# Kernel optimization log

Hardware: AMD Instinct MI355X
Metric: run time of the kernel (lower is better)

The kernel has to match this reference:

```python
import jax, jax.numpy as jnp
import numpy as np
import math

H = 16  # num heads
NEG = -1e9


def setup_inputs() -> dict:
    key = jax.random.key(0)
    ks = jax.random.split(key, 12)
    B, S, D = 2, 2048, 1024
    inp = {
        "query": jax.random.normal(ks[0], (B, S, D), jnp.float32),
        "key": jax.random.normal(ks[1], (B, S, D), jnp.float32),
        "value": jax.random.normal(ks[2], (B, S, D), jnp.float32),
        "mask": jax.random.randint(ks[3], (B, 1, S), 0, 2, jnp.int32),
        "wq": jax.random.normal(ks[4], (D, D), jnp.float32) * 0.02,
        "bq": jnp.zeros((D,), jnp.float32),
        "wk": jax.random.normal(ks[5], (D, D), jnp.float32) * 0.02,
        "bk": jnp.zeros((D,), jnp.float32),
        "wv": jax.random.normal(ks[6], (D, D), jnp.float32) * 0.02,
        "bv": jnp.zeros((D,), jnp.float32),
        "wo": jax.random.normal(ks[7], (D, D), jnp.float32) * 0.02,
        "bo": jnp.zeros((D,), jnp.float32),
    }
    return inp


def reference(query, key, value, mask, wq, bq, wk, bk, wv, bv, wo, bo):
    B, S, D = query.shape
    dk = D // H

    def proj(x, w, b):
        # torch Linear: x @ w.T + b ; then split heads -> [B, H, S, dk]
        y = x @ w.T + b
        return y.reshape(B, -1, H, dk).transpose(0, 2, 1, 3)

    q = proj(query, wq, bq)
    k = proj(key, wk, bk)
    v = proj(value, wv, bv)

    scores = jnp.einsum("bhqd,bhkd->bhqk", q, k) / math.sqrt(dk)  # [B,H,S,S]

    m = mask[:, None, :, :]  # [B,1,1,S] (mask.unsqueeze(1) in torch)
    scores = jnp.where(m == 0, NEG, scores)            # key-side padding mask
    scores = jnp.where(jnp.swapaxes(m, -2, -1) == 0, NEG, scores)  # query-side mask (q_len>1)

    p_attn = jax.nn.softmax(scores, axis=-1)
    # dropout p=0 / eval mode -> identity
    ctx = jnp.einsum("bhqk,bhkd->bhqd", p_attn, v)  # [B,H,S,dk]
    ctx = ctx.transpose(0, 2, 1, 3).reshape(B, S, H * dk)
    out = ctx @ wo.T + bo
    return out
```

## Files before the change

### kernel.cpp

```cpp
#include <hip/hip_runtime.h>
#include <hip/hip_bf16.h>

#define SEQ 2048
#define DIM 1024
#define NH  16
#define DK  64
#define NA  (2 * SEQ * DIM)
#define NW  (DIM * DIM)
#define PSTR 72
#define ESTR 136
#define FSTR 132
#define QSCALE 0.18033688011112042f

typedef __attribute__((ext_vector_type(4))) float f32x4;
typedef __attribute__((ext_vector_type(8))) __bf16 bf16x8;
typedef __attribute__((ext_vector_type(4))) __bf16 bf16x4;

__device__ __forceinline__ f32x4 mfma16(bf16x8 a, bf16x8 b, f32x4 c) {
  return __builtin_amdgcn_mfma_f32_16x16x32_bf16(a, b, c, 0, 0, 0);
}
__device__ __forceinline__ void async_load16(const void* g, void* l) {
  __builtin_amdgcn_global_load_lds(
      (const __attribute__((address_space(1))) void*)g,
      (__attribute__((address_space(3))) void*)l, 16, 0, 0);
}
__device__ __forceinline__ int swz(int row, int chunk) {
  return row * 8 + (chunk ^ (row & 7));
}

__global__ __launch_bounds__(256) void cvt_kernel(
    const float* __restrict__ s0, const float* __restrict__ s1,
    const float* __restrict__ s2, const float* __restrict__ s3,
    const float* __restrict__ s4, const float* __restrict__ s5,
    const float* __restrict__ s6,
    __hip_bfloat16* __restrict__ d0, __hip_bfloat16* __restrict__ d1,
    __hip_bfloat16* __restrict__ d2, __hip_bfloat16* __restrict__ d3,
    __hip_bfloat16* __restrict__ d4, __hip_bfloat16* __restrict__ d5,
    __hip_bfloat16* __restrict__ d6) {
  const int id = blockIdx.x;
  const float* s;
  __hip_bfloat16* d;
  int bid;
  if (id < 6144) {
    int t = id >> 11;
    bid = id & 2047;
    s = (t == 0) ? s0 : ((t == 1) ? s1 : s2);
    d = (t == 0) ? d0 : ((t == 1) ? d1 : d2);
  } else {
    int t = (id - 6144) >> 9;
    bid = (id - 6144) & 511;
    s = (t == 0) ? s3 : ((t == 1) ? s4 : ((t == 2) ? s5 : s6));
    d = (t == 0) ? d3 : ((t == 1) ? d4 : ((t == 2) ? d5 : d6));
  }
  size_t i = ((size_t)bid * 256 + threadIdx.x) * 8;
  float4 a = *(const float4*)(s + i);
  float4 b = *(const float4*)(s + i + 4);
  bf16x8 v = {(__bf16)a.x, (__bf16)a.y, (__bf16)a.z, (__bf16)a.w,
              (__bf16)b.x, (__bf16)b.y, (__bf16)b.z, (__bf16)b.w};
  *(bf16x8*)(d + i) = v;
}

__device__ __forceinline__ void gemm_mainloop(
    const __hip_bfloat16* __restrict__ X, const __hip_bfloat16* __restrict__ W,
    __hip_bfloat16* A_lds, __hip_bfloat16* B_lds, int m0, int n0,
    f32x4 acc[4][4]) {
  const int K = DIM;
  const int tid = threadIdx.x, lane = tid & 63, w = tid >> 6;
  const int quad = lane >> 4, l15 = lane & 15;
  const int wm = (w >> 1) * 64, wn = (w & 1) * 64;

  f32x4 z = {0.f, 0.f, 0.f, 0.f};
  for (int mi = 0; mi < 4; ++mi)
    for (int ni = 0; ni < 4; ++ni) acc[mi][ni] = z;

  for (int k0 = 0; k0 < K; k0 += 64) {
    for (int r = 0; r < 4; ++r) {
      int cbase = r * 256 + w * 64;
      int c = cbase + lane, row = c >> 3, cs = c & 7;
      int off = cs ^ (row & 7);
      async_load16((const char*)(X + (size_t)(m0 + row) * K + k0) + off * 16,
                   (char*)A_lds + cbase * 16);
      async_load16((const char*)(W + (size_t)(n0 + row) * K + k0) + off * 16,
                   (char*)B_lds + cbase * 16);
    }
    __syncthreads();
    for (int kk = 0; kk < 2; ++kk) {
      bf16x8 a[4], b[4];
      for (int mi = 0; mi < 4; ++mi)
        a[mi] = *(const bf16x8*)(A_lds + swz(wm + mi * 16 + l15, kk * 4 + quad) * 8);
      for (int ni = 0; ni < 4; ++ni)
        b[ni] = *(const bf16x8*)(B_lds + swz(wn + ni * 16 + l15, kk * 4 + quad) * 8);
      for (int mi = 0; mi < 4; ++mi)
        for (int ni = 0; ni < 4; ++ni)
          acc[mi][ni] = mfma16(a[mi], b[ni], acc[mi][ni]);
    }
    __syncthreads();
  }
}

__global__ __launch_bounds__(256) void qkv_proj_kernel(
    const __hip_bfloat16* __restrict__ xq, const __hip_bfloat16* __restrict__ xk,
    const __hip_bfloat16* __restrict__ xv,
    const __hip_bfloat16* __restrict__ wq, const __hip_bfloat16* __restrict__ wk,
    const __hip_bfloat16* __restrict__ wv,
    const float* __restrict__ bq, const float* __restrict__ bk,
    const float* __restrict__ bv,
    __hip_bfloat16* __restrict__ q_ws, __hip_bfloat16* __restrict__ k_ws,
    __hip_bfloat16* __restrict__ vt_ws) {
  __shared__ __align__(16) __hip_bfloat16 S_lds[128 * ESTR];

  const int z = blockIdx.z;
  const __hip_bfloat16* X = (z == 0) ? xq : ((z == 1) ? xk : xv);
  const __hip_bfloat16* W = (z == 0) ? wq : ((z == 1) ? wk : wv);
  const float* bias = (z == 0) ? bq : ((z == 1) ? bk : bv);
  const float f = (z == 0) ? QSCALE : 1.0f;

  const int m0 = blockIdx.y * 128, n0 = blockIdx.x * 128;
  f32x4 acc[4][4];
  gemm_mainloop(X, W, S_lds, S_lds + 128 * 64, m0, n0, acc);

  const int tid = threadIdx.x, lane = tid & 63, w = tid >> 6;
  const int quad = lane >> 4, l15 = lane & 15;
  const int wm = (w >> 1) * 64, wn = (w & 1) * 64;

  if (z != 2) {
    __hip_bfloat16* out = (z == 0) ? q_ws : k_ws;
    for (int p = 0; p < 2; ++p) {
      if ((w >> 1) == p) {
        for (int mi = 0; mi < 4; ++mi)
          for (int ni = 0; ni < 4; ++ni) {
            const float bv_ = bias[n0 + wn + ni * 16 + l15];
            for (int r = 0; r < 4; ++r)
              S_lds[(mi * 16 + quad * 4 + r) * ESTR + wn + ni * 16 + l15] =
                  __float2bfloat16((acc[mi][ni][r] + bv_) * f);
          }
      }
      __syncthreads();
      for (int r2 = 0; r2 < 4; ++r2) {
        int c = r2 * 256 + tid;
        int row = c >> 4, j = c & 15;
        int m = m0 + p * 64 + row, b = m >> 11, s = m & 2047;
        int n = n0 + j * 8, h = n >> 6, d = n & 63;
        *(uint4*)(out + ((size_t)(b * NH + h) * SEQ + s) * DK + d) =
            *(const uint4*)(S_lds + row * ESTR + j * 8);
      }
      __syncthreads();
    }
  } else {
    for (int mi = 0; mi < 4; ++mi)
      for (int ni = 0; ni < 4; ++ni) {
        const int n_local = wn + ni * 16 + l15;
        const float bv_ = bias[n0 + n_local];
        bf16x4 tv;
        for (int r = 0; r < 4; ++r) tv[r] = (__bf16)(acc[mi][ni][r] + bv_);
        *(bf16x4*)(S_lds + n_local * ESTR + wm + mi * 16 + quad * 4) = tv;
      }
    __syncthreads();
    const int b = m0 >> 11, s_base = m0 & 2047;
    for (int r2 = 0; r2 < 8; ++r2) {
      int c2 = r2 * 256 + tid;
      int nrow = c2 >> 4, moff = (c2 & 15) * 8;
      int n = n0 + nrow, h = n >> 6, d = n & 63;
      *(uint4*)(vt_ws + ((size_t)(b * NH + h) * DK + d) * SEQ + s_base + moff) =
          *(const uint4*)(S_lds + nrow * ESTR + moff);
    }
  }
}

__global__ __launch_bounds__(512) void attn_kernel(
    const __hip_bfloat16* __restrict__ qg, const __hip_bfloat16* __restrict__ kg,
    const __hip_bfloat16* __restrict__ vtg, const int* __restrict__ mask,
    __hip_bfloat16* __restrict__ ctx) {
  __shared__ __align__(16) __hip_bfloat16 QP_lds[128 * PSTR];
  __shared__ __align__(16) __hip_bfloat16 K_lds[2][64 * 64];
  __shared__ __align__(16) __hip_bfloat16 V_lds[2][64 * 64];
  __shared__ float bias_lds[SEQ];

  const int tid = threadIdx.x, lane = tid & 63, w = tid >> 6;
  const int quad = lane >> 4, l15 = lane & 15;
  const int bh = blockIdx.y, b = bh >> 4, h = bh & 15;
  const int q0 = blockIdx.x * 128;
  const size_t head = (size_t)bh * SEQ * DK;
  const size_t vthead = (size_t)bh * DK * SEQ;

  for (int i = tid; i < SEQ; i += 512)
    bias_lds[i] = mask[b * SEQ + i] ? 0.f : -1e9f;

  for (int r = 0; r < 2; ++r) {
    int cbase = r * 512 + w * 64;
    int c = cbase + lane, row = c >> 3, cs = c & 7;
    int off = cs ^ (row & 7);
    async_load16((const char*)(qg + head + (size_t)(q0 + row) * DK) + off * 16,
                 (char*)QP_lds + cbase * 16);
  }
  {
    int row = tid >> 3, cs = tid & 7;
    int off = cs ^ (row & 7);
    async_load16((const char*)(kg + head + (size_t)row * DK) + off * 16,
                 (char*)K_lds[0] + tid * 16);
    async_load16((const char*)(vtg + vthead + (size_t)row * SEQ) + off * 16,
                 (char*)V_lds[0] + tid * 16);
  }
  __syncthreads();

  bf16x8 qf[2];
  for (int kk = 0; kk < 2; ++kk)
    qf[kk] = *(const bf16x8*)(QP_lds + swz(w * 16 + l15, kk * 4 + quad) * 8);
  const int qmv = mask[b * SEQ + q0 + w * 16 + l15];

  __hip_bfloat16* P_lds = QP_lds;
  const bf16x8 ones = {(__bf16)1.f, (__bf16)1.f, (__bf16)1.f, (__bf16)1.f,
                       (__bf16)1.f, (__bf16)1.f, (__bf16)1.f, (__bf16)1.f};

  f32x4 z = {0.f, 0.f, 0.f, 0.f};
  f32x4 o_acc[4];
  for (int di = 0; di < 4; ++di) o_acc[di] = z;
  f32x4 o_sum = z;

  for (int t = 0; t < 32; ++t) {
    const int cur = t & 1;
    if (t < 31) {
      const int k1 = (t + 1) * 64;
      int row = tid >> 3, cs = tid & 7;
      int off = cs ^ (row & 7);
      async_load16((const char*)(kg + head + (size_t)(k1 + row) * DK) + off * 16,
                   (char*)K_lds[1 - cur] + tid * 16);
      async_load16((const char*)(vtg + vthead + (size_t)row * SEQ + k1) + off * 16,
                   (char*)V_lds[1 - cur] + tid * 16);
    }
    const int k0 = t * 64;

    f32x4 s_acc[4];
    for (int mi = 0; mi < 4; ++mi)
      s_acc[mi] = *(const f32x4*)(bias_lds + k0 + mi * 16 + quad * 4);
    for (int kk = 0; kk < 2; ++kk) {
      bf16x8 ak[4];
      for (int mi = 0; mi < 4; ++mi)
        ak[mi] = *(const bf16x8*)(K_lds[cur] + swz(mi * 16 + l15, kk * 4 + quad) * 8);
      for (int mi = 0; mi < 4; ++mi)
        s_acc[mi] = mfma16(ak[mi], qf[kk], s_acc[mi]);
    }

    for (int mi = 0; mi < 4; ++mi) {
      bf16x4 pk;
      for (int r = 0; r < 4; ++r) {
        float s2 = qmv ? s_acc[mi][r] : 0.f;
        pk[r] = (__bf16)__builtin_amdgcn_exp2f(s2);
      }
      *(bf16x4*)(P_lds + (w * 16 + l15) * PSTR + mi * 16 + quad * 4) = pk;
    }

    for (int kk = 0; kk < 2; ++kk) {
      bf16x8 bp = *(const bf16x8*)(P_lds + (w * 16 + l15) * PSTR + kk * 32 + quad * 8);
      bf16x8 av[4];
      for (int di = 0; di < 4; ++di)
        av[di] = *(const bf16x8*)(V_lds[cur] + swz(di * 16 + l15, kk * 4 + quad) * 8);
      for (int di = 0; di < 4; ++di)
        o_acc[di] = mfma16(av[di], bp, o_acc[di]);
      o_sum = mfma16(ones, bp, o_sum);
    }
    __syncthreads();
  }

  const float inv = 1.f / o_sum[0];

  for (int di = 0; di < 4; ++di) {
    bf16x4 ov;
    for (int r = 0; r < 4; ++r) ov[r] = (__bf16)(o_acc[di][r] * inv);
    *(bf16x4*)(P_lds + (w * 16 + l15) * PSTR + di * 16 + quad * 4) = ov;
  }
  __syncthreads();
  for (int r = 0; r < 2; ++r) {
    int c = r * 512 + tid, row = c >> 3, off = c & 7;
    *(uint4*)(ctx + (size_t)(b * SEQ + q0 + row) * DIM + h * DK + off * 8) =
        *(const uint4*)(P_lds + row * PSTR + off * 8);
  }
}

__global__ __launch_bounds__(256) void out_proj_kernel(
    const __hip_bfloat16* __restrict__ ctx, const __hip_bfloat16* __restrict__ wo,
    const float* __restrict__ bo, float* __restrict__ out) {
  __shared__ __align__(16) __hip_bfloat16 S_lds[64 * FSTR * 2];

  const int m0 = blockIdx.y * 128, n0 = blockIdx.x * 128;
  f32x4 acc[4][4];
  gemm_mainloop(ctx, wo, S_lds, S_lds + 128 * 64, m0, n0, acc);

  const int tid = threadIdx.x, lane = tid & 63, w = tid >> 6;
  const int quad = lane >> 4, l15 = lane & 15;
  const int wn = (w & 1) * 64;
  float* epi = (float*)S_lds;

  for (int p = 0; p < 2; ++p) {
    if ((w >> 1) == p) {
      for (int mi = 0; mi < 4; ++mi)
        for (int ni = 0; ni < 4; ++ni) {
          const float bv_ = bo[n0 + wn + ni * 16 + l15];
          for (int r = 0; r < 4; ++r)
            epi[(mi * 16 + quad * 4 + r) * FSTR + wn + ni * 16 + l15] =
                acc[mi][ni][r] + bv_;
        }
    }
    __syncthreads();
    for (int r2 = 0; r2 < 8; ++r2) {
      int c = r2 * 256 + tid;
      int row = c >> 5, j = c & 31;
      *(float4*)(out + (size_t)(m0 + p * 64 + row) * DIM + n0 + j * 4) =
          *(const float4*)(epi + row * FSTR + j * 4);
    }
    __syncthreads();
  }
}

extern "C" void kernel_launch(void* const* d_in, const int* in_sizes, int n_in,
                              void* d_out, int out_size, void* d_ws, size_t ws_size,
                              hipStream_t stream) {
  const float* query = (const float*)d_in[0];
  const float* key   = (const float*)d_in[1];
  const float* value = (const float*)d_in[2];
  const int*   mask  = (const int*)d_in[3];
  const float* wq = (const float*)d_in[4];
  const float* bq = (const float*)d_in[5];
  const float* wk = (const float*)d_in[6];
  const float* bk = (const float*)d_in[7];
  const float* wv = (const float*)d_in[8];
  const float* bv = (const float*)d_in[9];
  const float* wo = (const float*)d_in[10];
  const float* bo = (const float*)d_in[11];
  float* out = (float*)d_out;

  char* ws = (char*)d_ws;
  const size_t SZA = (size_t)NA * 2;
  const size_t SZW = (size_t)NW * 2;
  __hip_bfloat16* xq  = (__hip_bfloat16*)(ws);
  __hip_bfloat16* xk  = (__hip_bfloat16*)(ws + SZA);
  __hip_bfloat16* xv  = (__hip_bfloat16*)(ws + 2 * SZA);
  __hip_bfloat16* wqb = (__hip_bfloat16*)(ws + 3 * SZA);
  __hip_bfloat16* wkb = (__hip_bfloat16*)(ws + 3 * SZA + SZW);
  __hip_bfloat16* wvb = (__hip_bfloat16*)(ws + 3 * SZA + 2 * SZW);
  __hip_bfloat16* wob = (__hip_bfloat16*)(ws + 3 * SZA + 3 * SZW);
  __hip_bfloat16* q_ws  = (__hip_bfloat16*)(ws + 3 * SZA + 4 * SZW);
  __hip_bfloat16* k_ws  = (__hip_bfloat16*)(ws + 4 * SZA + 4 * SZW);
  __hip_bfloat16* vt_ws = (__hip_bfloat16*)(ws + 5 * SZA + 4 * SZW);
  __hip_bfloat16* ctx_ws = xq;

  cvt_kernel<<<dim3(8192), dim3(256), 0, stream>>>(
      query, key, value, wq, wk, wv, wo, xq, xk, xv, wqb, wkb, wvb, wob);
  qkv_proj_kernel<<<dim3(8, 32, 3), dim3(256), 0, stream>>>(
      xq, xk, xv, wqb, wkb, wvb, bq, bk, bv, q_ws, k_ws, vt_ws);
  attn_kernel<<<dim3(16, 32), dim3(512), 0, stream>>>(q_ws, k_ws, vt_ws, mask, ctx_ws);
  out_proj_kernel<<<dim3(8, 32), dim3(256), 0, stream>>>(ctx_ws, wob, bo, out);
}
```

Before: 238.5 us.

## Double-buffer GEMM LDS tiles and single-pass epilogues in projection kernels

The shared GEMM mainloop now prefetches the next K-tile into a second LDS buffer with async global-to-LDS loads while MFMAs run on the current buffer, replacing the load-sync-compute serialization. The QKV and output projection epilogues stage the full 128x128 tile in LDS at once instead of two half passes, which removes extra barriers. This grows LDS use per block (to about 64–68KB), which may reduce how many blocks fit per CU.

```diff
diff --git a/kernel.cpp b/kernel.cpp
--- a/kernel.cpp
+++ b/kernel.cpp
@@ -60,11 +60,24 @@
   *(bf16x8*)(d + i) = v;
 }
 
+__device__ __forceinline__ void gemm_stage(
+    const __hip_bfloat16* __restrict__ X, const __hip_bfloat16* __restrict__ W,
+    __hip_bfloat16* A, __hip_bfloat16* B, int m0, int n0, int k0,
+    int w, int lane) {
+  for (int r = 0; r < 4; ++r) {
+    int cbase = r * 256 + w * 64;
+    int c = cbase + lane, row = c >> 3, cs = c & 7;
+    int off = cs ^ (row & 7);
+    async_load16((const char*)(X + (size_t)(m0 + row) * DIM + k0) + off * 16,
+                 (char*)A + cbase * 16);
+    async_load16((const char*)(W + (size_t)(n0 + row) * DIM + k0) + off * 16,
+                 (char*)B + cbase * 16);
+  }
+}
+
 __device__ __forceinline__ void gemm_mainloop(
     const __hip_bfloat16* __restrict__ X, const __hip_bfloat16* __restrict__ W,
-    __hip_bfloat16* A_lds, __hip_bfloat16* B_lds, int m0, int n0,
-    f32x4 acc[4][4]) {
-  const int K = DIM;
+    __hip_bfloat16* lds, int m0, int n0, f32x4 acc[4][4]) {
   const int tid = threadIdx.x, lane = tid & 63, w = tid >> 6;
   const int quad = lane >> 4, l15 = lane & 15;
   const int wm = (w >> 1) * 64, wn = (w & 1) * 64;
@@ -73,23 +86,22 @@
   for (int mi = 0; mi < 4; ++mi)
     for (int ni = 0; ni < 4; ++ni) acc[mi][ni] = z;
 
-  for (int k0 = 0; k0 < K; k0 += 64) {
-    for (int r = 0; r < 4; ++r) {
-      int cbase = r * 256 + w * 64;
-      int c = cbase + lane, row = c >> 3, cs = c & 7;
-      int off = cs ^ (row & 7);
-      async_load16((const char*)(X + (size_t)(m0 + row) * K + k0) + off * 16,
-                   (char*)A_lds + cbase * 16);
-      async_load16((const char*)(W + (size_t)(n0 + row) * K + k0) + off * 16,
-                   (char*)B_lds + cbase * 16);
-    }
-    __syncthreads();
+  gemm_stage(X, W, lds, lds + 8192, m0, n0, 0, w, lane);
+  __syncthreads();
+
+  for (int it = 0; it < 16; ++it) {
+    __hip_bfloat16* Ac = lds + (it & 1) * 16384;
+    __hip_bfloat16* Bc = Ac + 8192;
+    if (it < 15) {
+      __hip_bfloat16* An = lds + ((it + 1) & 1) * 16384;
+      gemm_stage(X, W, An, An + 8192, m0, n0, (it + 1) * 64, w, lane);
+    }
     for (int kk = 0; kk < 2; ++kk) {
       bf16x8 a[4], b[4];
       for (int mi = 0; mi < 4; ++mi)
-        a[mi] = *(const bf16x8*)(A_lds + swz(wm + mi * 16 + l15, kk * 4 + quad) * 8);
+        a[mi] = *(const bf16x8*)(Ac + swz(wm + mi * 16 + l15, kk * 4 + quad) * 8);
       for (int ni = 0; ni < 4; ++ni)
-        b[ni] = *(const bf16x8*)(B_lds + swz(wn + ni * 16 + l15, kk * 4 + quad) * 8);
+        b[ni] = *(const bf16x8*)(Bc + swz(wn + ni * 16 + l15, kk * 4 + quad) * 8);
       for (int mi = 0; mi < 4; ++mi)
         for (int ni = 0; ni < 4; ++ni)
           acc[mi][ni] = mfma16(a[mi], b[ni], acc[mi][ni]);
@@ -107,7 +119,7 @@
     const float* __restrict__ bv,
     __hip_bfloat16* __restrict__ q_ws, __hip_bfloat16* __restrict__ k_ws,
     __hip_bfloat16* __restrict__ vt_ws) {
-  __shared__ __align__(16) __hip_bfloat16 S_lds[128 * ESTR];
+  __shared__ __align__(16) __hip_bfloat16 S_lds[4 * 8192];
 
   const int z = blockIdx.z;
   const __hip_bfloat16* X = (z == 0) ? xq : ((z == 1) ? xk : xv);
@@ -117,7 +129,7 @@
 
   const int m0 = blockIdx.y * 128, n0 = blockIdx.x * 128;
   f32x4 acc[4][4];
-  gemm_mainloop(X, W, S_lds, S_lds + 128 * 64, m0, n0, acc);
+  gemm_mainloop(X, W, S_lds, m0, n0, acc);
 
   const int tid = threadIdx.x, lane = tid & 63, w = tid >> 6;
   const int quad = lane >> 4, l15 = lane & 15;
@@ -125,26 +137,21 @@
 
   if (z != 2) {
     __hip_bfloat16* out = (z == 0) ? q_ws : k_ws;
-    for (int p = 0; p < 2; ++p) {
-      if ((w >> 1) == p) {
-        for (int mi = 0; mi < 4; ++mi)
-          for (int ni = 0; ni < 4; ++ni) {
-            const float bv_ = bias[n0 + wn + ni * 16 + l15];
-            for (int r = 0; r < 4; ++r)
-              S_lds[(mi * 16 + quad * 4 + r) * ESTR + wn + ni * 16 + l15] =
-                  __float2bfloat16((acc[mi][ni][r] + bv_) * f);
-          }
+    for (int mi = 0; mi < 4; ++mi)
+      for (int ni = 0; ni < 4; ++ni) {
+        const float bv_ = bias[n0 + wn + ni * 16 + l15];
+        for (int r = 0; r < 4; ++r)
+          S_lds[(wm + mi * 16 + quad * 4 + r) * ESTR + wn + ni * 16 + l15] =
+              __float2bfloat16((acc[mi][ni][r] + bv_) * f);
       }
-      __syncthreads();
-      for (int r2 = 0; r2 < 4; ++r2) {
-        int c = r2 * 256 + tid;
-        int row = c >> 4, j = c & 15;
-        int m = m0 + p * 64 + row, b = m >> 11, s = m & 2047;
-        int n = n0 + j * 8, h = n >> 6, d = n & 63;
-        *(uint4*)(out + ((size_t)(b * NH + h) * SEQ + s) * DK + d) =
-            *(const uint4*)(S_lds + row * ESTR + j * 8);
-      }
-      __syncthreads();
+    __syncthreads();
+    for (int r2 = 0; r2 < 8; ++r2) {
+      int c = r2 * 256 + tid;
+      int row = c >> 4, j = c & 15;
+      int m = m0 + row, b = m >> 11, s = m & 2047;
+      int n = n0 + j * 8, h = n >> 6, d = n & 63;
+      *(uint4*)(out + ((size_t)(b * NH + h) * SEQ + s) * DK + d) =
+          *(const uint4*)(S_lds + row * ESTR + j * 8);
     }
   } else {
     for (int mi = 0; mi < 4; ++mi)
@@ -280,35 +287,31 @@
 __global__ __launch_bounds__(256) void out_proj_kernel(
     const __hip_bfloat16* __restrict__ ctx, const __hip_bfloat16* __restrict__ wo,
     const float* __restrict__ bo, float* __restrict__ out) {
-  __shared__ __align__(16) __hip_bfloat16 S_lds[64 * FSTR * 2];
+  __shared__ __align__(16) char S_raw[128 * FSTR * 4];
+  __hip_bfloat16* S_lds = (__hip_bfloat16*)S_raw;
 
   const int m0 = blockIdx.y * 128, n0 = blockIdx.x * 128;
   f32x4 acc[4][4];
-  gemm_mainloop(ctx, wo, S_lds, S_lds + 128 * 64, m0, n0, acc);
+  gemm_mainloop(ctx, wo, S_lds, m0, n0, acc);
 
   const int tid = threadIdx.x, lane = tid & 63, w = tid >> 6;
   const int quad = lane >> 4, l15 = lane & 15;
-  const int wn = (w & 1) * 64;
-  float* epi = (float*)S_lds;
-
-  for (int p = 0; p < 2; ++p) {
-    if ((w >> 1) == p) {
-      for (int mi = 0; mi < 4; ++mi)
-        for (int ni = 0; ni < 4; ++ni) {
-          const float bv_ = bo[n0 + wn + ni * 16 + l15];
-          for (int r = 0; r < 4; ++r)
-            epi[(mi * 16 + quad * 4 + r) * FSTR + wn + ni * 16 + l15] =
-                acc[mi][ni][r] + bv_;
-        }
-    }
-    __syncthreads();
-    for (int r2 = 0; r2 < 8; ++r2) {
-      int c = r2 * 256 + tid;
-      int row = c >> 5, j = c & 31;
-      *(float4*)(out + (size_t)(m0 + p * 64 + row) * DIM + n0 + j * 4) =
-          *(const float4*)(epi + row * FSTR + j * 4);
-    }
-    __syncthreads();
+  const int wm = (w >> 1) * 64, wn = (w & 1) * 64;
+  float* epi = (float*)S_raw;
+
+  for (int mi = 0; mi < 4; ++mi)
+    for (int ni = 0; ni < 4; ++ni) {
+      const float bv_ = bo[n0 + wn + ni * 16 + l15];
+      for (int r = 0; r < 4; ++r)
+        epi[(wm + mi * 16 + quad * 4 + r) * FSTR + wn + ni * 16 + l15] =
+            acc[mi][ni][r] + bv_;
+    }
+  __syncthreads();
+  for (int r2 = 0; r2 < 16; ++r2) {
+    int c = r2 * 256 + tid;
+    int row = c >> 5, j = c & 31;
+    *(float4*)(out + (size_t)(m0 + row) * DIM + n0 + j * 4) =
+        *(const float4*)(epi + row * FSTR + j * 4);
   }
 }
 
```

Result: faster. 225.9 us (-5.3%).
